# Performance work log

Measured on AMD Instinct MI355X. Metric: run time of the kernel, lower is better.

## Reference

```python
import jax, jax.numpy as jnp
import numpy as np

N_NODES = 50000
N_EDGES = 800000
D_IN = 128
D_HID = 128
N_LAYERS = 3
BN_EPS = 1e-5


def setup_inputs() -> dict:
    key = jax.random.key(0)
    ks = jax.random.split(key, 12)
    x = jax.random.normal(ks[0], (N_NODES, D_IN), dtype=jnp.float32)
    edge_index = jax.random.randint(ks[1], (2, N_EDGES), 0, N_NODES, dtype=jnp.int64)
    edge_weight = jax.random.uniform(ks[2], (N_EDGES,), dtype=jnp.float32)
    s1 = 1.0 / np.sqrt(D_IN)
    s2 = 1.0 / np.sqrt(D_HID)
    # stacked per-layer GIN MLP params (layer 0 in_dim == hidden_dim so stacking is valid)
    W1s = jax.random.uniform(ks[3], (N_LAYERS, D_HID, D_HID), jnp.float32, -s1, s1)
    b1s = jax.random.uniform(ks[4], (N_LAYERS, D_HID), jnp.float32, -s1, s1)
    W2s = jax.random.uniform(ks[5], (N_LAYERS, D_HID, D_HID), jnp.float32, -s2, s2)
    b2s = jax.random.uniform(ks[6], (N_LAYERS, D_HID), jnp.float32, -s2, s2)
    eps = jnp.zeros((N_LAYERS,), jnp.float32)  # GINConv eps init 0
    gamma = jnp.ones((D_HID,), jnp.float32)
    beta = jnp.zeros((D_HID,), jnp.float32)
    Wp = jax.random.uniform(ks[7], (D_HID, D_HID), jnp.float32, -s2, s2)
    bp = jax.random.uniform(ks[8], (D_HID,), jnp.float32, -s2, s2)
    prelu_a = jnp.asarray(0.25, jnp.float32)
    return {"x": x, "edge_weight": edge_weight, "W1s": W1s, "b1s": b1s,
            "W2s": W2s, "b2s": b2s, "eps": eps, "gamma": gamma, "beta": beta,
            "Wp": Wp, "bp": bp, "prelu_a": prelu_a, "edge_index": edge_index}


def reference(x, edge_weight, W1s, b1s, W2s, b2s, eps, gamma, beta, Wp, bp, prelu_a, edge_index):
    src, dst = edge_index[0], edge_index[1]
    z = x
    for i in range(N_LAYERS):
        # GINConv: sum-aggregate weighted neighbor messages, then 2-layer MLP
        msg = z[src] * edge_weight[:, None]                       # [E, d]
        agg = jax.ops.segment_sum(msg, dst, num_segments=N_NODES)  # [N, d]
        h = (1.0 + eps[i]) * z + agg
        h = jax.nn.relu(h @ W1s[i] + b1s[i]) @ W2s[i] + b2s[i]
        z = jax.nn.relu(h)  # activation; dropout inactive (eval)
    # BatchNorm1d (training-mode batch statistics, biased variance)
    mean = jnp.mean(z, axis=0)
    var = jnp.var(z, axis=0)
    zn = (z - mean) * jax.lax.rsqrt(var + BN_EPS) * gamma + beta
    # projection head: Linear -> PReLU (dropout inactive)
    p = zn @ Wp + bp
    p = jnp.where(p >= 0, p, prelu_a * p)
    return zn, p
```

## Files before the change

### kernel.cpp

```cpp
#include <hip/hip_runtime.h>
#include <hip/hip_fp16.h>

#define N_NODES 50000
#define N_EDGES 800000
#define D 128
#define ND (N_NODES * D)
#define BN_EPS 1e-5f

#define NB 256
#define NPB 196
#define BCAP 4096

typedef short bf16x8 __attribute__((ext_vector_type(8)));
typedef _Float16 f16x8 __attribute__((ext_vector_type(8)));
typedef float f32x4 __attribute__((ext_vector_type(4)));
typedef unsigned short u16x8 __attribute__((ext_vector_type(8)));

__device__ inline unsigned short f2bf(float f) {
    unsigned int u = __float_as_uint(f);
    u += 0x7FFF + ((u >> 16) & 1);
    return (unsigned short)(u >> 16);
}
__device__ inline float bf2f(unsigned short h) {
    return __uint_as_float(((unsigned int)h) << 16);
}
__device__ inline unsigned short f2h(float f) {
    return __half_as_ushort(__float2half(f));
}
__device__ inline float h2f(unsigned short u) {
    return __half2float(__ushort_as_half(u));
}
__device__ inline f16x8 as_f16x8(u16x8 v) {
    union { u16x8 u; f16x8 f; } x; x.u = v; return x.f;
}

__global__ void convert_x(const float* __restrict__ x, ushort* __restrict__ xh) {
    int i = (blockIdx.x * blockDim.x + threadIdx.x) * 4;
    if (i < ND) {
        float4 v = *(const float4*)(x + i);
        *(ushort4*)(xh + i) = make_ushort4(f2h(v.x), f2h(v.y), f2h(v.z), f2h(v.w));
    }
}

__global__ void pack_w_split(const float* __restrict__ W1s, const float* __restrict__ W2s,
                             const float* __restrict__ Wp, ushort* __restrict__ out) {
    int idx = blockIdx.x * blockDim.x + threadIdx.x;
    if (idx >= 7 * 16384) return;
    int m = idx >> 14;
    int p = idx & 16383;
    int c = p >> 11;
    int kc = (p >> 9) & 3;
    int lane = (p >> 3) & 63;
    int j = p & 7;
    int k = kc * 32 + (lane >> 4) * 8 + j;
    int col = c * 16 + (lane & 15);
    const float* src = (m < 3) ? (W1s + (size_t)m * 16384)
                     : (m < 6) ? (W2s + (size_t)(m - 3) * 16384)
                               : Wp;
    float v = src[k * 128 + col];
    if (m < 3) {
        unsigned short hi = f2h(v);
        float r = (v - h2f(hi)) * 2048.0f;
        out[(size_t)(2 * m) * 16384 + p] = hi;
        out[(size_t)(2 * m + 1) * 16384 + p] = f2h(r);
    } else {
        unsigned short hi = f2bf(v);
        float r = v - bf2f(hi);
        out[(size_t)(2 * m) * 16384 + p] = hi;
        out[(size_t)(2 * m + 1) * 16384 + p] = f2bf(r);
    }
}

__global__ void hist_kernel(const int* __restrict__ dst, int* __restrict__ offs) {
    int e = blockIdx.x * blockDim.x + threadIdx.x;
    if (e < N_EDGES) atomicAdd(&offs[dst[e] + 1], 1);
}

__global__ void scan_kernel(int* __restrict__ offs, int* __restrict__ bcur) {
    __shared__ int wsum[16];
    __shared__ int carry_s;
    int tid = threadIdx.x;
    int lane = tid & 63;
    int wave = tid >> 6;
    if (tid == 0) carry_s = 0;
    __syncthreads();
    for (int base = 1; base <= N_NODES; base += 8192) {
        int i0 = base + tid * 8;
        int v[8];
        #pragma unroll
        for (int k = 0; k < 8; ++k) {
            int idx = i0 + k;
            v[k] = (idx <= N_NODES) ? offs[idx] : 0;
        }
        #pragma unroll
        for (int k = 1; k < 8; ++k) v[k] += v[k - 1];
        int tsum = v[7];
        int x = tsum;
        #pragma unroll
        for (int d = 1; d < 64; d <<= 1) {
            int y = __shfl_up(x, d, 64);
            if (lane >= d) x += y;
        }
        if (lane == 63) wsum[wave] = x;
        __syncthreads();
        if (wave == 0 && lane < 16) {
            int y = wsum[lane];
            #pragma unroll
            for (int d = 1; d < 16; d <<= 1) {
                int t = __shfl_up(y, d, 64);
                if (lane >= d) y += t;
            }
            wsum[lane] = y;
        }
        __syncthreads();
        int waveoff = (wave > 0) ? wsum[wave - 1] : 0;
        int total = wsum[15];
        int add = (x - tsum) + waveoff + carry_s;
        #pragma unroll
        for (int k = 0; k < 8; ++k) {
            int idx = i0 + k;
            if (idx <= N_NODES) offs[idx] = v[k] + add;
        }
        __syncthreads();
        if (tid == 0) carry_s += total;
        __syncthreads();
    }
    if (tid < NB) bcur[tid] = offs[tid * NPB];
}

__global__ __launch_bounds__(256) void bucket_scatter(
    const int* __restrict__ src, const int* __restrict__ dst,
    const float* __restrict__ ew, int* __restrict__ bcur,
    uint2* __restrict__ pay) {
    __shared__ int cnt[NB];
    __shared__ int cur[NB];
    int tid = threadIdx.x;
    for (int i = tid; i < NB; i += 256) cnt[i] = 0;
    __syncthreads();
    int base = blockIdx.x * 2048;
    int s[8], d[8], b[8];
    float w[8];
    #pragma unroll
    for (int k = 0; k < 8; ++k) {
        int e = base + k * 256 + tid;
        bool v = e < N_EDGES;
        d[k] = v ? dst[e] : 0;
        s[k] = v ? src[e] : 0;
        w[k] = v ? ew[e] : 0.f;
        b[k] = d[k] / NPB;
        if (v) atomicAdd(&cnt[b[k]], 1);
    }
    __syncthreads();
    for (int i = tid; i < NB; i += 256) {
        int c = cnt[i];
        cur[i] = (c > 0) ? atomicAdd(&bcur[i], c) : 0;
    }
    __syncthreads();
    #pragma unroll
    for (int k = 0; k < 8; ++k) {
        int e = base + k * 256 + tid;
        if (e < N_EDGES) {
            int bk = b[k];
            int p = atomicAdd(&cur[bk], 1);
            unsigned dloc = (unsigned)(d[k] - bk * NPB);
            pay[p] = make_uint2((unsigned)s[k] | (dloc << 17), __float_as_uint(w[k]));
        }
    }
}

__global__ __launch_bounds__(256) void bucket_sort(const int* __restrict__ offs,
                                                   uint2* __restrict__ pay) {
    __shared__ uint2 lp[BCAP];
    __shared__ int cur[NPB];
    int b = blockIdx.x;
    int tid = threadIdx.x;
    int n0 = b * NPB;
    int n1 = min(n0 + NPB, N_NODES);
    int nn = n1 - n0;
    int r0 = offs[n0];
    int r1 = offs[n1];
    for (int i = tid; i < nn; i += 256) cur[i] = offs[n0 + i] - r0;
    __syncthreads();
    int cnt = r1 - r0;
    for (int i = tid; i < cnt; i += 256) {
        uint2 e = pay[r0 + i];
        int dloc = (int)(e.x >> 17);
        int p = atomicAdd(&cur[dloc], 1);
        if (p < BCAP) lp[p] = make_uint2(e.x & 0x1FFFFu, e.y);
    }
    __syncthreads();
    for (int i = tid; i < cnt; i += 256) {
        if (i < BCAP) pay[r0 + i] = lp[i];
    }
}

__global__ void gather_agg_f16(const ushort* __restrict__ z, const int* __restrict__ offs,
                               const uint2* __restrict__ pay,
                               const float* __restrict__ epsp, int layer,
                               ushort* __restrict__ A) {
    int tid = blockIdx.x * blockDim.x + threadIdx.x;
    int n = tid >> 5;
    if (n >= N_NODES) return;
    int f = (tid & 31) << 2;
    float epsv = 1.0f + epsp[layer];
    int beg = offs[n], end = offs[n + 1];
    ushort4 zi = *(const ushort4*)(z + (size_t)n * D + f);
    float ax = epsv * h2f(zi.x), ay = epsv * h2f(zi.y);
    float az = epsv * h2f(zi.z), aw = epsv * h2f(zi.w);
    int j = beg;
    for (; j + 4 <= end; j += 4) {
        uint2 e0 = pay[j];
        uint2 e1 = pay[j + 1];
        uint2 e2 = pay[j + 2];
        uint2 e3 = pay[j + 3];
        ushort4 v0 = *(const ushort4*)(z + (size_t)e0.x * D + f);
        ushort4 v1 = *(const ushort4*)(z + (size_t)e1.x * D + f);
        ushort4 v2 = *(const ushort4*)(z + (size_t)e2.x * D + f);
        ushort4 v3 = *(const ushort4*)(z + (size_t)e3.x * D + f);
        float w0 = __uint_as_float(e0.y);
        float w1 = __uint_as_float(e1.y);
        float w2 = __uint_as_float(e2.y);
        float w3 = __uint_as_float(e3.y);
        ax += h2f(v0.x) * w0 + h2f(v1.x) * w1 + h2f(v2.x) * w2 + h2f(v3.x) * w3;
        ay += h2f(v0.y) * w0 + h2f(v1.y) * w1 + h2f(v2.y) * w2 + h2f(v3.y) * w3;
        az += h2f(v0.z) * w0 + h2f(v1.z) * w1 + h2f(v2.z) * w2 + h2f(v3.z) * w3;
        aw += h2f(v0.w) * w0 + h2f(v1.w) * w1 + h2f(v2.w) * w2 + h2f(v3.w) * w3;
    }
    for (; j < end; ++j) {
        uint2 e0 = pay[j];
        ushort4 v0 = *(const ushort4*)(z + (size_t)e0.x * D + f);
        float w0 = __uint_as_float(e0.y);
        ax += h2f(v0.x) * w0; ay += h2f(v0.y) * w0;
        az += h2f(v0.z) * w0; aw += h2f(v0.w) * w0;
    }
    *(ushort4*)(A + (size_t)n * D + f) = make_ushort4(f2h(ax), f2h(ay), f2h(az), f2h(aw));
}

#define HSTR 132
template<bool STATS>
__global__ __launch_bounds__(256) void mlp_fused(
    const ushort* __restrict__ A,
    const ushort* __restrict__ W1hi, const ushort* __restrict__ W1lo,
    const float* __restrict__ b1,
    const ushort* __restrict__ W2hi, const ushort* __restrict__ W2lo,
    const float* __restrict__ b2, ushort* __restrict__ Z,
    float* __restrict__ stats) {
    __shared__ float Hs[64 * HSTR];
    int tid = threadIdx.x;
    int lane = tid & 63;
    int wave = tid >> 6;
    int rlo = lane & 15;
    int quad = lane >> 4;
    int blk0 = blockIdx.x * 64;

    const f16x8* W1h = (const f16x8*)W1hi;
    const f16x8* W1l = (const f16x8*)W1lo;
    const bf16x8* W2h = (const bf16x8*)W2hi;
    const bf16x8* W2l = (const bf16x8*)W2lo;

    f16x8 af[4][4];
    #pragma unroll
    for (int rf = 0; rf < 4; ++rf) {
        int arow = blk0 + rf * 16 + rlo;
        int ar = (arow < N_NODES) ? arow : (N_NODES - 1);
        #pragma unroll
        for (int kc = 0; kc < 4; ++kc) {
            u16x8 raw = *(const u16x8*)(A + (size_t)ar * D + kc * 32 + quad * 8);
            af[rf][kc] = as_f16x8(raw);
        }
    }

    #pragma unroll
    for (int cc = 0; cc < 2; ++cc) {
        int c = 2 * wave + cc;
        f32x4 aH[4], aL[4];
        #pragma unroll
        for (int rf = 0; rf < 4; ++rf) {
            aH[rf] = (f32x4){0.f, 0.f, 0.f, 0.f};
            aL[rf] = (f32x4){0.f, 0.f, 0.f, 0.f};
        }
        #pragma unroll
        for (int kc = 0; kc < 4; ++kc) {
            f16x8 wh = W1h[(c * 4 + kc) * 64 + lane];
            f16x8 wl = W1l[(c * 4 + kc) * 64 + lane];
            #pragma unroll
            for (int rf = 0; rf < 4; ++rf) {
                aH[rf] = __builtin_amdgcn_mfma_f32_16x16x32_f16(af[rf][kc], wh, aH[rf], 0, 0, 0);
                aL[rf] = __builtin_amdgcn_mfma_f32_16x16x32_f16(af[rf][kc], wl, aL[rf], 0, 0, 0);
            }
        }
        int col = c * 16 + rlo;
        float bb = b1[col];
        #pragma unroll
        for (int rf = 0; rf < 4; ++rf) {
            #pragma unroll
            for (int r = 0; r < 4; ++r) {
                Hs[(rf * 16 + quad * 4 + r) * HSTR + col] =
                    fmaxf(aH[rf][r] + aL[rf][r] * (1.0f / 2048.0f) + bb, 0.f);
            }
        }
    }
    __syncthreads();

    f32x4 acc2[2][4];
    #pragma unroll
    for (int cc = 0; cc < 2; ++cc)
        #pragma unroll
        for (int rf = 0; rf < 4; ++rf)
            acc2[cc][rf] = (f32x4){0.f, 0.f, 0.f, 0.f};

    #pragma unroll
    for (int kc = 0; kc < 4; ++kc) {
        bf16x8 a2hi[4], a2lo[4];
        #pragma unroll
        for (int rf = 0; rf < 4; ++rf) {
            const float* p = &Hs[(rf * 16 + rlo) * HSTR + kc * 32 + quad * 8];
            #pragma unroll
            for (int j = 0; j < 8; ++j) {
                float v = p[j];
                unsigned short h = f2bf(v);
                a2hi[rf][j] = (short)h;
                a2lo[rf][j] = (short)f2bf(v - bf2f(h));
            }
        }
        #pragma unroll
        for (int cc = 0; cc < 2; ++cc) {
            int c = 2 * wave + cc;
            bf16x8 wh = W2h[(c * 4 + kc) * 64 + lane];
            bf16x8 wl = W2l[(c * 4 + kc) * 64 + lane];
            #pragma unroll
            for (int rf = 0; rf < 4; ++rf) {
                acc2[cc][rf] = __builtin_amdgcn_mfma_f32_16x16x32_bf16(a2lo[rf], wh, acc2[cc][rf], 0, 0, 0);
                acc2[cc][rf] = __builtin_amdgcn_mfma_f32_16x16x32_bf16(a2hi[rf], wl, acc2[cc][rf], 0, 0, 0);
                acc2[cc][rf] = __builtin_amdgcn_mfma_f32_16x16x32_bf16(a2hi[rf], wh, acc2[cc][rf], 0, 0, 0);
            }
        }
    }
    __syncthreads();

    #pragma unroll
    for (int cc = 0; cc < 2; ++cc) {
        int c = 2 * wave + cc;
        int col = c * 16 + rlo;
        float bb = b2[col];
        float s = 0.f, s2 = 0.f;
        #pragma unroll
        for (int rf = 0; rf < 4; ++rf) {
            #pragma unroll
            for (int r = 0; r < 4; ++r) {
                float v = fmaxf(acc2[cc][rf][r] + bb, 0.f);
                Hs[(rf * 16 + quad * 4 + r) * HSTR + col] = v;
                if (STATS) {
                    float m = (blk0 + rf * 16 + quad * 4 + r < N_NODES) ? v : 0.f;
                    s += m;
                    s2 += m * m;
                }
            }
        }
        if (STATS) {
            s  += __shfl_xor(s, 16, 64);
            s  += __shfl_xor(s, 32, 64);
            s2 += __shfl_xor(s2, 16, 64);
            s2 += __shfl_xor(s2, 32, 64);
            if (quad == 0) {
                atomicAdd(&stats[col], s);
                atomicAdd(&stats[D + col], s2);
            }
        }
    }
    __syncthreads();

    #pragma unroll
    for (int it = 0; it < 4; ++it) {
        int r = wave * 16 + it * 4 + quad;
        int grow = blk0 + r;
        if (grow < N_NODES) {
            const float* p = &Hs[r * HSTR + rlo * 8];
            float4 lo = *(const float4*)p;
            float4 hi = *(const float4*)(p + 4);
            ushort us[8] = {f2h(lo.x), f2h(lo.y), f2h(lo.z), f2h(lo.w),
                            f2h(hi.x), f2h(hi.y), f2h(hi.z), f2h(hi.w)};
            *(float4*)(Z + (size_t)grow * D + rlo * 8) = *(const float4*)us;
        }
    }
}

#define PSTR 132
__global__ __launch_bounds__(256) void bn_proj(
    const ushort* __restrict__ Z, const float* __restrict__ stats,
    const float* __restrict__ gamma, const float* __restrict__ beta,
    const ushort* __restrict__ Wphi, const ushort* __restrict__ Wplo,
    const float* __restrict__ bp, const float* __restrict__ prelu_a,
    float* __restrict__ zn_out, float* __restrict__ p_out) {
    __shared__ float sc_s[D];
    __shared__ float sh_s[D];
    __shared__ float Ps[4][16 * PSTR];
    int tid = threadIdx.x;
    int lane = tid & 63;
    int wave = tid >> 6;
    int rlo = lane & 15;
    int quad = lane >> 4;

    if (tid < D) {
        float m = stats[tid] * (1.0f / N_NODES);
        float v = stats[D + tid] * (1.0f / N_NODES) - m * m;
        float rs = rsqrtf(v + BN_EPS);
        float sc = rs * gamma[tid];
        sc_s[tid] = sc;
        sh_s[tid] = beta[tid] - m * sc;
    }
    __syncthreads();

    int row0 = blockIdx.x * 64 + wave * 16;
    int arow = row0 + rlo;
    int ar = (arow < N_NODES) ? arow : (N_NODES - 1);

    const bf16x8* Wh = (const bf16x8*)Wphi;
    const bf16x8* Wl = (const bf16x8*)Wplo;

    bf16x8 ahi[4], alo[4];
    #pragma unroll
    for (int kc = 0; kc < 4; ++kc) {
        u16x8 raw = *(const u16x8*)(Z + (size_t)ar * D + kc * 32 + quad * 8);
        float zn[8];
        #pragma unroll
        for (int j = 0; j < 8; ++j) {
            int k = kc * 32 + quad * 8 + j;
            zn[j] = sc_s[k] * h2f(raw[j]) + sh_s[k];
            unsigned short h = f2bf(zn[j]);
            ahi[kc][j] = (short)h;
            alo[kc][j] = (short)f2bf(zn[j] - bf2f(h));
        }
        if (arow < N_NODES) {
            float* dst = zn_out + (size_t)arow * D + kc * 32 + quad * 8;
            *(float4*)dst = make_float4(zn[0], zn[1], zn[2], zn[3]);
            *(float4*)(dst + 4) = make_float4(zn[4], zn[5], zn[6], zn[7]);
        }
    }

    f32x4 acc[8];
    #pragma unroll
    for (int c = 0; c < 8; ++c) acc[c] = (f32x4){0.f, 0.f, 0.f, 0.f};
    #pragma unroll
    for (int c = 0; c < 8; ++c) {
        #pragma unroll
        for (int kc = 0; kc < 4; ++kc) {
            bf16x8 wh = Wh[(c * 4 + kc) * 64 + lane];
            bf16x8 wl = Wl[(c * 4 + kc) * 64 + lane];
            acc[c] = __builtin_amdgcn_mfma_f32_16x16x32_bf16(alo[kc], wh, acc[c], 0, 0, 0);
            acc[c] = __builtin_amdgcn_mfma_f32_16x16x32_bf16(ahi[kc], wl, acc[c], 0, 0, 0);
            acc[c] = __builtin_amdgcn_mfma_f32_16x16x32_bf16(ahi[kc], wh, acc[c], 0, 0, 0);
        }
    }

    float aP = prelu_a[0];
    #pragma unroll
    for (int c = 0; c < 8; ++c) {
        int col = c * 16 + rlo;
        float bb = bp[col];
        #pragma unroll
        for (int r = 0; r < 4; ++r) {
            float v = acc[c][r] + bb;
            v = (v >= 0.f) ? v : aP * v;
            Ps[wave][(quad * 4 + r) * PSTR + col] = v;
        }
    }
    __syncthreads();
    #pragma unroll
    for (int p2 = 0; p2 < 8; ++p2) {
        int r = p2 * 2 + (lane >> 5);
        int grow = row0 + r;
        if (grow < N_NODES) {
            *(float4*)(p_out + (size_t)grow * D + (lane & 31) * 4) =
                *(const float4*)&Ps[wave][r * PSTR + (lane & 31) * 4];
        }
    }
}

extern "C" void kernel_launch(void* const* d_in, const int* in_sizes, int n_in,
                              void* d_out, int out_size, void* d_ws, size_t ws_size,
                              hipStream_t stream) {
    (void)in_sizes; (void)n_in; (void)out_size; (void)ws_size;
    const float* x     = (const float*)d_in[0];
    const float* ew    = (const float*)d_in[1];
    const float* W1s   = (const float*)d_in[2];
    const float* b1s   = (const float*)d_in[3];
    const float* W2s   = (const float*)d_in[4];
    const float* b2s   = (const float*)d_in[5];
    const float* eps   = (const float*)d_in[6];
    const float* gamma = (const float*)d_in[7];
    const float* beta  = (const float*)d_in[8];
    const float* Wp    = (const float*)d_in[9];
    const float* bp    = (const float*)d_in[10];
    const float* pa    = (const float*)d_in[11];
    const int*   ei    = (const int*)d_in[12];
    const int* srcp = ei;
    const int* dstp = ei + N_EDGES;

    char* wsb = (char*)d_ws;
    float*  stats  = (float*)wsb;                 wsb += 1024;
    int*    offs   = (int*)wsb;                   wsb += 200016;
    int*    bcur   = (int*)wsb;                   wsb += 200016;
    uint2*  pay    = (uint2*)wsb;                 wsb += 6400000;
    ushort* Wpk    = (ushort*)wsb;                wsb += 14 * 16384 * 2;
    ushort* Xh     = (ushort*)wsb;                wsb += (size_t)ND * 2;
    ushort* Ah     = (ushort*)wsb;                wsb += (size_t)ND * 2;
    ushort* Zh     = (ushort*)wsb;                wsb += (size_t)ND * 2;

    float* out_zn = (float*)d_out;
    float* out_p  = out_zn + ND;

    hipMemsetAsync(stats, 0, 256 * sizeof(float), stream);
    hipMemsetAsync(offs, 0, (N_NODES + 1) * sizeof(int), stream);

    convert_x<<<(ND / 4 + 255) / 256, 256, 0, stream>>>(x, Xh);
    pack_w_split<<<(7 * 16384 + 255) / 256, 256, 0, stream>>>(W1s, W2s, Wp, Wpk);

    hist_kernel<<<(N_EDGES + 255) / 256, 256, 0, stream>>>(dstp, offs);
    scan_kernel<<<1, 1024, 0, stream>>>(offs, bcur);
    bucket_scatter<<<(N_EDGES + 2047) / 2048, 256, 0, stream>>>(srcp, dstp, ew, bcur, pay);
    bucket_sort<<<NB, 256, 0, stream>>>(offs, pay);

    int mgrid = (N_NODES + 63) / 64;
    const ushort* zin = Xh;
    for (int l = 0; l < 3; ++l) {
        gather_agg_f16<<<(N_NODES * 32 + 255) / 256, 256, 0, stream>>>(zin, offs, pay, eps, l, Ah);
        if (l < 2) {
            mlp_fused<false><<<mgrid, 256, 0, stream>>>(Ah,
                Wpk + (size_t)(2 * l) * 16384,       Wpk + (size_t)(2 * l + 1) * 16384, b1s + (size_t)l * D,
                Wpk + (size_t)(2 * (3 + l)) * 16384, Wpk + (size_t)(2 * (3 + l) + 1) * 16384, b2s + (size_t)l * D,
                Zh, stats);
        } else {
            mlp_fused<true><<<mgrid, 256, 0, stream>>>(Ah,
                Wpk + (size_t)(2 * l) * 16384,       Wpk + (size_t)(2 * l + 1) * 16384, b1s + (size_t)l * D,
                Wpk + (size_t)(2 * (3 + l)) * 16384, Wpk + (size_t)(2 * (3 + l) + 1) * 16384, b2s + (size_t)l * D,
                Zh, stats);
        }
        zin = Zh;
    }
    bn_proj<<<mgrid, 256, 0, stream>>>(Zh, stats, gamma, beta,
        Wpk + (size_t)12 * 16384, Wpk + (size_t)13 * 16384, bp, pa, out_zn, out_p);
}
```

Baseline: 404.3 us.

## Replace per-node histogram and serial scan with bucket-level counts; store MLP hidden as bf16 hi/lo

The CSR build no longer runs global per-node atomics and a single-block 50k-element scan. It counts edges per bucket with shared-memory atomics, scans only 256 bucket totals, and computes per-node offsets inside bucket_sort through a local histogram and scan. Separately, the MLP intermediate is written to shared memory already split into bf16 hi/lo halves, so the second GEMM loads vectors without repeated conversion, and the output is kept as f16 in shared memory. This adds block scans inside bucket_sort, and bucket_sort's per-node offsets are only correct if each bucket spans at most 256 nodes, which holds since NPB is 196.

```diff
diff --git a/kernel.cpp b/kernel.cpp
--- a/kernel.cpp
+++ b/kernel.cpp
@@ -32,6 +32,9 @@
 }
 __device__ inline f16x8 as_f16x8(u16x8 v) {
     union { u16x8 u; f16x8 f; } x; x.u = v; return x.f;
+}
+__device__ inline bf16x8 as_bf16x8(u16x8 v) {
+    union { u16x8 u; bf16x8 f; } x; x.u = v; return x.f;
 }
 
 __global__ void convert_x(const float* __restrict__ x, ushort* __restrict__ xh) {
@@ -71,61 +74,41 @@
     }
 }
 
-__global__ void hist_kernel(const int* __restrict__ dst, int* __restrict__ offs) {
-    int e = blockIdx.x * blockDim.x + threadIdx.x;
-    if (e < N_EDGES) atomicAdd(&offs[dst[e] + 1], 1);
-}
-
-__global__ void scan_kernel(int* __restrict__ offs, int* __restrict__ bcur) {
-    __shared__ int wsum[16];
-    __shared__ int carry_s;
+__global__ __launch_bounds__(256) void bhist_kernel(const int* __restrict__ dst,
+                                                    int* __restrict__ gbcnt) {
+    __shared__ int cnt[NB];
     int tid = threadIdx.x;
-    int lane = tid & 63;
-    int wave = tid >> 6;
-    if (tid == 0) carry_s = 0;
-    __syncthreads();
-    for (int base = 1; base <= N_NODES; base += 8192) {
-        int i0 = base + tid * 8;
-        int v[8];
-        #pragma unroll
-        for (int k = 0; k < 8; ++k) {
-            int idx = i0 + k;
-            v[k] = (idx <= N_NODES) ? offs[idx] : 0;
-        }
-        #pragma unroll
-        for (int k = 1; k < 8; ++k) v[k] += v[k - 1];
-        int tsum = v[7];
-        int x = tsum;
-        #pragma unroll
-        for (int d = 1; d < 64; d <<= 1) {
-            int y = __shfl_up(x, d, 64);
-            if (lane >= d) x += y;
-        }
-        if (lane == 63) wsum[wave] = x;
+    cnt[tid] = 0;
+    __syncthreads();
+    int base = blockIdx.x * 2048;
+    #pragma unroll
+    for (int k = 0; k < 8; ++k) {
+        int e = base + k * 256 + tid;
+        if (e < N_EDGES) atomicAdd(&cnt[dst[e] / NPB], 1);
+    }
+    __syncthreads();
+    int c = cnt[tid];
+    if (c > 0) atomicAdd(&gbcnt[tid], c);
+}
+
+__global__ __launch_bounds__(256) void bscan_kernel(const int* __restrict__ gbcnt,
+                                                    int* __restrict__ bstart,
+                                                    int* __restrict__ bcur) {
+    __shared__ int s[NB];
+    int tid = threadIdx.x;
+    int v = gbcnt[tid];
+    s[tid] = v;
+    __syncthreads();
+    for (int d = 1; d < NB; d <<= 1) {
+        int t = (tid >= d) ? s[tid - d] : 0;
         __syncthreads();
-        if (wave == 0 && lane < 16) {
-            int y = wsum[lane];
-            #pragma unroll
-            for (int d = 1; d < 16; d <<= 1) {
-                int t = __shfl_up(y, d, 64);
-                if (lane >= d) y += t;
-            }
-            wsum[lane] = y;
-        }
+        s[tid] += t;
         __syncthreads();
-        int waveoff = (wave > 0) ? wsum[wave - 1] : 0;
-        int total = wsum[15];
-        int add = (x - tsum) + waveoff + carry_s;
-        #pragma unroll
-        for (int k = 0; k < 8; ++k) {
-            int idx = i0 + k;
-            if (idx <= N_NODES) offs[idx] = v[k] + add;
-        }
-        __syncthreads();
-        if (tid == 0) carry_s += total;
-        __syncthreads();
-    }
-    if (tid < NB) bcur[tid] = offs[tid * NPB];
+    }
+    int incl = s[tid];
+    bstart[tid] = incl - v;
+    bcur[tid] = incl - v;
+    if (tid == NB - 1) bstart[NB] = incl;
 }
 
 __global__ __launch_bounds__(256) void bucket_scatter(
@@ -168,29 +151,48 @@
     }
 }
 
-__global__ __launch_bounds__(256) void bucket_sort(const int* __restrict__ offs,
+__global__ __launch_bounds__(256) void bucket_sort(const int* __restrict__ bstart,
+                                                   int* __restrict__ offs,
                                                    uint2* __restrict__ pay) {
     __shared__ uint2 lp[BCAP];
+    __shared__ int lcnt[NB];
     __shared__ int cur[NPB];
     int b = blockIdx.x;
     int tid = threadIdx.x;
     int n0 = b * NPB;
     int n1 = min(n0 + NPB, N_NODES);
     int nn = n1 - n0;
-    int r0 = offs[n0];
-    int r1 = offs[n1];
-    for (int i = tid; i < nn; i += 256) cur[i] = offs[n0 + i] - r0;
-    __syncthreads();
+    int r0 = bstart[b];
+    int r1 = bstart[b + 1];
     int cnt = r1 - r0;
+    lcnt[tid] = 0;
+    __syncthreads();
     for (int i = tid; i < cnt; i += 256) {
         uint2 e = pay[r0 + i];
-        int dloc = (int)(e.x >> 17);
-        int p = atomicAdd(&cur[dloc], 1);
-        if (p < BCAP) lp[p] = make_uint2(e.x & 0x1FFFFu, e.y);
-    }
+        if (i < BCAP) lp[i] = e;
+        atomicAdd(&lcnt[e.x >> 17], 1);
+    }
+    __syncthreads();
+    int v = lcnt[tid];
+    for (int d = 1; d < NB; d <<= 1) {
+        int t = (tid >= d) ? lcnt[tid - d] : 0;
+        __syncthreads();
+        lcnt[tid] += t;
+        __syncthreads();
+    }
+    int excl = lcnt[tid] - v;
+    if (tid < nn) {
+        offs[n0 + tid] = r0 + excl;
+        cur[tid] = excl;
+    }
+    if (tid == 0) offs[n1] = r1;
     __syncthreads();
     for (int i = tid; i < cnt; i += 256) {
-        if (i < BCAP) pay[r0 + i] = lp[i];
+        if (i < BCAP) {
+            uint2 e = lp[i];
+            int p = atomicAdd(&cur[e.x >> 17], 1);
+            if (p < BCAP) pay[r0 + p] = make_uint2(e.x & 0x1FFFFu, e.y);
+        }
     }
 }
 
@@ -236,7 +238,7 @@
     *(ushort4*)(A + (size_t)n * D + f) = make_ushort4(f2h(ax), f2h(ay), f2h(az), f2h(aw));
 }
 
-#define HSTR 132
+#define HSTR2 136
 template<bool STATS>
 __global__ __launch_bounds__(256) void mlp_fused(
     const ushort* __restrict__ A,
@@ -245,7 +247,8 @@
     const ushort* __restrict__ W2hi, const ushort* __restrict__ W2lo,
     const float* __restrict__ b2, ushort* __restrict__ Z,
     float* __restrict__ stats) {
-    __shared__ float Hs[64 * HSTR];
+    __shared__ ushort Hhi[64 * HSTR2];
+    __shared__ ushort Hlo[64 * HSTR2];
     int tid = threadIdx.x;
     int lane = tid & 63;
     int wave = tid >> 6;
@@ -295,8 +298,11 @@
         for (int rf = 0; rf < 4; ++rf) {
             #pragma unroll
             for (int r = 0; r < 4; ++r) {
-                Hs[(rf * 16 + quad * 4 + r) * HSTR + col] =
-                    fmaxf(aH[rf][r] + aL[rf][r] * (1.0f / 2048.0f) + bb, 0.f);
+                float v = fmaxf(aH[rf][r] + aL[rf][r] * (1.0f / 2048.0f) + bb, 0.f);
+                unsigned short h = f2bf(v);
+                int idx = (rf * 16 + quad * 4 + r) * HSTR2 + col;
+                Hhi[idx] = h;
+                Hlo[idx] = f2bf(v - bf2f(h));
             }
         }
     }
@@ -314,14 +320,9 @@
         bf16x8 a2hi[4], a2lo[4];
         #pragma unroll
         for (int rf = 0; rf < 4; ++rf) {
-            const float* p = &Hs[(rf * 16 + rlo) * HSTR + kc * 32 + quad * 8];
-            #pragma unroll
-            for (int j = 0; j < 8; ++j) {
-                float v = p[j];
-                unsigned short h = f2bf(v);
-                a2hi[rf][j] = (short)h;
-                a2lo[rf][j] = (short)f2bf(v - bf2f(h));
-            }
+            int idx = (rf * 16 + rlo) * HSTR2 + kc * 32 + quad * 8;
+            a2hi[rf] = as_bf16x8(*(const u16x8*)&Hhi[idx]);
+            a2lo[rf] = as_bf16x8(*(const u16x8*)&Hlo[idx]);
         }
         #pragma unroll
         for (int cc = 0; cc < 2; ++cc) {
@@ -349,7 +350,7 @@
             #pragma unroll
             for (int r = 0; r < 4; ++r) {
                 float v = fmaxf(acc2[cc][rf][r] + bb, 0.f);
-                Hs[(rf * 16 + quad * 4 + r) * HSTR + col] = v;
+                Hhi[(rf * 16 + quad * 4 + r) * HSTR2 + col] = f2h(v);
                 if (STATS) {
                     float m = (blk0 + rf * 16 + quad * 4 + r < N_NODES) ? v : 0.f;
                     s += m;
@@ -375,12 +376,8 @@
         int r = wave * 16 + it * 4 + quad;
         int grow = blk0 + r;
         if (grow < N_NODES) {
-            const float* p = &Hs[r * HSTR + rlo * 8];
-            float4 lo = *(const float4*)p;
-            float4 hi = *(const float4*)(p + 4);
-            ushort us[8] = {f2h(lo.x), f2h(lo.y), f2h(lo.z), f2h(lo.w),
-                            f2h(hi.x), f2h(hi.y), f2h(hi.z), f2h(hi.w)};
-            *(float4*)(Z + (size_t)grow * D + rlo * 8) = *(const float4*)us;
+            u16x8 vv = *(const u16x8*)&Hhi[r * HSTR2 + rlo * 8];
+            *(u16x8*)(Z + (size_t)grow * D + rlo * 8) = vv;
         }
     }
 }
@@ -500,7 +497,9 @@
     char* wsb = (char*)d_ws;
     float*  stats  = (float*)wsb;                 wsb += 1024;
     int*    offs   = (int*)wsb;                   wsb += 200016;
-    int*    bcur   = (int*)wsb;                   wsb += 200016;
+    int*    bcur   = (int*)wsb;
+    int*    gbcnt  = bcur + 256;
+    int*    bstart = bcur + 512;                  wsb += 200016;
     uint2*  pay    = (uint2*)wsb;                 wsb += 6400000;
     ushort* Wpk    = (ushort*)wsb;                wsb += 14 * 16384 * 2;
     ushort* Xh     = (ushort*)wsb;                wsb += (size_t)ND * 2;
@@ -511,15 +510,15 @@
     float* out_p  = out_zn + ND;
 
     hipMemsetAsync(stats, 0, 256 * sizeof(float), stream);
-    hipMemsetAsync(offs, 0, (N_NODES + 1) * sizeof(int), stream);
+    hipMemsetAsync(gbcnt, 0, NB * sizeof(int), stream);
 
     convert_x<<<(ND / 4 + 255) / 256, 256, 0, stream>>>(x, Xh);
     pack_w_split<<<(7 * 16384 + 255) / 256, 256, 0, stream>>>(W1s, W2s, Wp, Wpk);
 
-    hist_kernel<<<(N_EDGES + 255) / 256, 256, 0, stream>>>(dstp, offs);
-    scan_kernel<<<1, 1024, 0, stream>>>(offs, bcur);
+    bhist_kernel<<<(N_EDGES + 2047) / 2048, 256, 0, stream>>>(dstp, gbcnt);
+    bscan_kernel<<<1, 256, 0, stream>>>(gbcnt, bstart, bcur);
     bucket_scatter<<<(N_EDGES + 2047) / 2048, 256, 0, stream>>>(srcp, dstp, ew, bcur, pay);
-    bucket_sort<<<NB, 256, 0, stream>>>(offs, pay);
+    bucket_sort<<<NB, 256, 0, stream>>>(bstart, offs, pay);
 
     int mgrid = (N_NODES + 63) / 64;
     const ushort* zin = Xh;
```

New measurement: 371.1 us. 8.2% less time.
